# Kernel optimization log

Hardware: AMD Instinct MI355X
Metric: run time of the kernel (lower is better)

The kernel has to match this reference:

```python
import jax, jax.numpy as jnp
import numpy as np

NEG = -1e30  # safe -inf surrogate for log-space DP
BLANK = 0    # torch.nn.CTCLoss default blank index


def _ctc_loss_sum(lp, labels, in_lens, lab_lens):
    """CTC negative log-likelihood, summed over batch.
    lp: [T, B, V] log-probabilities; labels: [B, L] int; in_lens, lab_lens: [B] int.
    """
    T, B, V = lp.shape
    L = labels.shape[1]
    S = 2 * L + 1  # extended label length (blanks interleaved)
    s = jnp.arange(S)
    # extended label sequence z: blank at even positions, label at odd
    ext = jnp.where(s % 2 == 0, BLANK, labels[:, jnp.clip((s - 1) // 2, 0, L - 1)])  # [B,S]
    ext_m2 = jnp.concatenate([jnp.full((B, 2), BLANK, ext.dtype), ext[:, :-2]], axis=1)
    skip = (s >= 2) & (ext != BLANK) & (ext != ext_m2)  # [B,S] skip-transition allowed
    # emission log-probs gathered at extended labels: [T,B,S]
    emit = jnp.take_along_axis(lp, jnp.broadcast_to(ext[None], (T, B, S)), axis=2)
    alpha0 = jnp.full((B, S), NEG, lp.dtype)
    alpha0 = alpha0.at[:, 0].set(emit[0, :, 0]).at[:, 1].set(emit[0, :, 1])

    def step(alpha, inputs):
        emit_t, t = inputs
        a1 = jnp.concatenate([jnp.full((B, 1), NEG, alpha.dtype), alpha[:, :-1]], axis=1)
        a2 = jnp.concatenate([jnp.full((B, 2), NEG, alpha.dtype), alpha[:, :-2]], axis=1)
        comb = jnp.logaddexp(alpha, a1)
        comb = jnp.where(skip, jnp.logaddexp(comb, a2), comb)
        new = comb + emit_t
        # past each sequence's length, freeze alpha
        new = jnp.where(t < in_lens[:, None], new, alpha)
        return new, None

    alpha, _ = jax.lax.scan(step, alpha0, (emit[1:], jnp.arange(1, T)))
    s_last = 2 * lab_lens  # final blank position per sample
    bidx = jnp.arange(B)
    ll = jnp.logaddexp(alpha[bidx, s_last], alpha[bidx, s_last - 1])
    return jnp.sum(-ll)


def setup_inputs() -> dict:
    key = jax.random.key(0)
    k1, k2, k3, k4, k5, k6 = jax.random.split(key, 6)
    B, T, H, V, L = 16, 512, 512, 4096, 64
    hs_pad = jax.random.normal(k1, (B, T, H), dtype=jnp.float32)
    hs_lens = jax.random.randint(k2, (B,), T // 2, T + 1, dtype=jnp.int32)
    ys_pad = jax.random.randint(k3, (B, L), 1, V, dtype=jnp.int32)  # avoid blank=0
    ys_lens = jax.random.randint(k4, (B,), L // 2, L + 1, dtype=jnp.int32)
    W = jax.random.normal(k5, (H, V), dtype=jnp.float32) * (H ** -0.5)
    b = jax.random.normal(k6, (V,), dtype=jnp.float32) * 0.01
    return {"hs_pad": hs_pad, "hs_lens": hs_lens, "ys_pad": ys_pad,
            "ys_lens": ys_lens, "W": W, "b": b}


def reference(hs_pad, hs_lens, ys_pad, ys_lens, W, b):
    # projection (dropout_rate=0.0 -> identity) + log_softmax
    logits = jnp.einsum('bth,hv->btv', hs_pad, W) + b
    log_probs = jax.nn.log_softmax(logits, axis=-1)
    lp = jnp.transpose(log_probs, (1, 0, 2))  # [T,B,V]
    B = lp.shape[1]
    loss = _ctc_loss_sum(lp, ys_pad, hs_lens, ys_lens)
    return loss / B
```

## Files before the change

kernel.cpp:

```cpp
#include <hip/hip_runtime.h>
#include <hip/hip_bf16.h>
#include <math.h>

#define BB   16
#define TT   512
#define HH   512
#define VV   4096
#define LL   64
#define SS   129
#define JJ   65
#define MM   (BB*TT)

#define LOG2E 1.4426950408889634f
#define LN2   0.6931471805599453f

typedef __bf16 bf16;
typedef __attribute__((ext_vector_type(4))) __bf16 bf16x4;
typedef __attribute__((ext_vector_type(8))) __bf16 bf16x8;
typedef __attribute__((ext_vector_type(4))) float f32x4;

template<int CTRL>
__device__ __forceinline__ float dpp_mov(float x) {
    return __int_as_float(__builtin_amdgcn_update_dpp(
        __float_as_int(x), __float_as_int(x), CTRL, 0xF, 0xF, false));
}
__device__ __forceinline__ float row16_max(float x) {
    x = fmaxf(x, dpp_mov<0x128>(x));
    x = fmaxf(x, dpp_mov<0x124>(x));
    x = fmaxf(x, dpp_mov<0x122>(x));
    x = fmaxf(x, dpp_mov<0x121>(x));
    return x;
}
__device__ __forceinline__ float row16_sum(float x) {
    x += dpp_mov<0x128>(x);
    x += dpp_mov<0x124>(x);
    x += dpp_mov<0x122>(x);
    x += dpp_mov<0x121>(x);
    return x;
}
__device__ __forceinline__ float dpp_shr1_zero(float x) {
    int r = __builtin_amdgcn_update_dpp(0, __float_as_int(x),
                                        0x138 , 0xF, 0xF, false);
    return __int_as_float(r);
}
template<int CTRL>
__device__ __forceinline__ float dpp_max_t(float m) {
    int r = __builtin_amdgcn_update_dpp(0, __float_as_int(m), CTRL, 0xF, 0xF, false);
    return fmaxf(m, __int_as_float(r));
}

__global__ __launch_bounds__(256) void prep(const float* __restrict__ hs,
                                            const float* __restrict__ W,
                                            bf16* __restrict__ Abf,
                                            bf16* __restrict__ Wt)
{
    __shared__ float t[64][65];
    const int tid = threadIdx.x;
    int bx = blockIdx.x;
    if (bx < 4096) {
        int idx = bx * 256 + tid;
        float4 v = ((const float4*)hs)[idx];
        bf16x4 o = {(bf16)v.x, (bf16)v.y, (bf16)v.z, (bf16)v.w};
        *(bf16x4*)(Abf + (size_t)idx * 4) = o;
    } else {
        bx -= 4096;
        const int n0 = (bx & 63) * 64;
        const int k0 = (bx >> 6) * 64;
        #pragma unroll
        for (int i = 0; i < 16; ++i) {
            int idx = tid + i * 256;
            int kk = idx >> 6, nn = idx & 63;
            t[kk][nn] = W[(size_t)(k0 + kk) * VV + n0 + nn];
        }
        __syncthreads();
        #pragma unroll
        for (int i = 0; i < 16; ++i) {
            int idx = tid + i * 256;
            int nl = idx >> 6, kk = idx & 63;
            Wt[(size_t)(n0 + nl) * HH + k0 + kk] = (bf16)t[kk][nl];
        }
    }
}

#define TN 128
#define NT64 (VV / 64)

#define GLDS(src, dst) \
    __builtin_amdgcn_global_load_lds((const __attribute__((address_space(1))) void*)(src), \
                                     (__attribute__((address_space(3))) void*)(dst), 16, 0, 0)

__global__ __launch_bounds__(256) void gemm_lse_mfma(
    const bf16* __restrict__ A,
    const bf16* __restrict__ Bt,
    const float* __restrict__ bias,
    const int*  __restrict__ ys,
    float* __restrict__ part,
    float* __restrict__ glpT)
{
    __shared__ bf16 As[128 * 32];
    __shared__ bf16 Bs[128 * 32];
    const int tid = threadIdx.x;
    const int lane = tid & 63;
    const int wid = tid >> 6;
    const int wm = wid >> 1, wn = wid & 1;
    const int m0 = blockIdx.y * 128, n0 = blockIdx.x * 128;
    const int lq = lane & 15, kg = lane >> 4;

    f32x4 acc[4][4];
    const f32x4 z = {0.f, 0.f, 0.f, 0.f};
    #pragma unroll
    for (int i = 0; i < 4; ++i)
        #pragma unroll
        for (int j = 0; j < 4; ++j) acc[i][j] = z;

    const int c0 = tid;
    const int row0 = c0 >> 2, sl0 = (c0 & 3) ^ (row0 & 3);
    const int c1 = tid + 256;
    const int row1 = c1 >> 2, sl1 = (c1 & 3) ^ (row1 & 3);
    bf16* dstA0 = As + (size_t)(0 * 256 + (tid & 192)) * 8;
    bf16* dstA1 = As + (size_t)(1 * 256 + (tid & 192)) * 8;
    bf16* dstB0 = Bs + (size_t)(0 * 256 + (tid & 192)) * 8;
    bf16* dstB1 = Bs + (size_t)(1 * 256 + (tid & 192)) * 8;
    const bf16* srcA0 = A  + (size_t)(m0 + row0) * HH + sl0 * 8;
    const bf16* srcA1 = A  + (size_t)(m0 + row1) * HH + sl1 * 8;
    const bf16* srcB0 = Bt + (size_t)(n0 + row0) * HH + sl0 * 8;
    const bf16* srcB1 = Bt + (size_t)(n0 + row1) * HH + sl1 * 8;

    for (int k0 = 0; k0 < HH; k0 += 32) {
        GLDS(srcA0 + k0, dstA0);
        GLDS(srcA1 + k0, dstA1);
        GLDS(srcB0 + k0, dstB0);
        GLDS(srcB1 + k0, dstB1);
        __syncthreads();
        bf16x8 a[4], b[4];
        #pragma unroll
        for (int i = 0; i < 4; ++i) {
            int ar = wm * 64 + i * 16 + lq;
            a[i] = *(const bf16x8*)&As[ar * 32 + ((kg ^ (ar & 3)) * 8)];
        }
        #pragma unroll
        for (int j = 0; j < 4; ++j) {
            int br = wn * 64 + j * 16 + lq;
            b[j] = *(const bf16x8*)&Bs[br * 32 + ((kg ^ (br & 3)) * 8)];
        }
        #pragma unroll
        for (int i = 0; i < 4; ++i)
            #pragma unroll
            for (int j = 0; j < 4; ++j)
                acc[i][j] = __builtin_amdgcn_mfma_f32_16x16x32_bf16(a[i], b[j], acc[i][j], 0, 0, 0);
        __syncthreads();
    }

    const int ct = blockIdx.x * 2 + wn;
    float bj[4];
    #pragma unroll
    for (int j = 0; j < 4; ++j) bj[j] = bias[n0 + wn * 64 + j * 16 + lq];
    #pragma unroll
    for (int i = 0; i < 4; ++i) {
        #pragma unroll
        for (int r = 0; r < 4; ++r) {
            float v[4], mx = -3.4e38f;
            #pragma unroll
            for (int j = 0; j < 4; ++j) { v[j] = acc[i][j][r] + bj[j]; mx = fmaxf(mx, v[j]); }
            mx = row16_max(mx);
            float sm = 0.f;
            #pragma unroll
            for (int j = 0; j < 4; ++j) sm += __expf(v[j] - mx);
            sm = row16_sum(sm);
            if (lq == 0) {
                int rowg = m0 + wm * 64 + i * 16 + kg * 4 + r;
                size_t o = ((size_t)rowg * NT64 + ct) * 2;
                part[o] = mx; part[o + 1] = sm;
            }
        }
    }

    const int bidx = m0 >> 9;
    const int t0s  = (m0 & 511) + wm * 64;
    const int nbase = n0 + wn * 64;
    for (int j = 0; j < JJ; ++j) {
        int c = (j == 0) ? 0 : ys[bidx * LL + j - 1];
        int local = c - nbase;
        if (local >= 0 && local < 64) {
            int cl = local & 15;
            float bc = bias[c];
            #pragma unroll
            for (int jt = 0; jt < 4; ++jt) {
                if ((local >> 4) == jt && lq == cl) {
                    #pragma unroll
                    for (int i = 0; i < 4; ++i)
                        #pragma unroll
                        for (int r = 0; r < 4; ++r) {
                            int tt = t0s + i * 16 + kg * 4 + r;
                            glpT[(size_t)(bidx * JJ + j) * TT + tt] = acc[i][jt][r] + bc;
                        }
                }
            }
        }
    }
}

__global__ __launch_bounds__(256) void lse_merge(const float* __restrict__ part,
                                                 float* __restrict__ lse)
{
    const int lane = threadIdx.x & 63;
    const int r = blockIdx.x * 4 + (threadIdx.x >> 6);
    const float* p = part + (size_t)r * (NT64 * 2);
    float mx = p[2 * lane];
    float sm = p[2 * lane + 1];
    float wmax = mx;
    #pragma unroll
    for (int d = 1; d < 64; d <<= 1) wmax = fmaxf(wmax, __shfl_xor(wmax, d));
    float c = sm * __expf(mx - wmax);
    #pragma unroll
    for (int d = 1; d < 64; d <<= 1) c += __shfl_xor(c, d);
    if (lane == 0) lse[r] = wmax + logf(c);
}

#define F4AT(arr, u) ( ((u) & 3) == 0 ? arr[(u) >> 2].x \
                     : ((u) & 3) == 1 ? arr[(u) >> 2].y \
                     : ((u) & 3) == 2 ? arr[(u) >> 2].z : arr[(u) >> 2].w )

#define LOADI(p0v, pBv, blk) { \
    int bb_ = (blk); bb_ = bb_ < 32 ? bb_ : 31; \
    const float4* p0_ = (const float4*)(g0 + bb_ * 16); \
    const float4* pB_ = (const float4*)(gB + bb_ * 16); \
    p0v[0] = p0_[0]; p0v[1] = p0_[1]; p0v[2] = p0_[2]; p0v[3] = p0_[3]; \
    pBv[0] = pB_[0]; pBv[1] = pB_[1]; pBv[2] = pB_[2]; pBv[3] = pB_[3]; \
}

#define RVCOMP(rv, p0v, pBv, blk) { \
    const int tB_ = (blk) * 16; \
    _Pragma("unroll") \
    for (int u = 0; u < 16; ++u) { \
        rv[u] = __builtin_amdgcn_exp2f((F4AT(pBv, u) - F4AT(p0v, u)) * LOG2E); \
    } \
    if (tB_ > 0 && tB_ + 16 <= Tin) { \
        float s_ = 0.f; \
        _Pragma("unroll") \
        for (int u = 0; u < 16; ++u) s_ += F4AT(p0v, u); \
        corr += s_; \
    } else { \
        float s_ = 0.f; \
        _Pragma("unroll") \
        for (int u = 0; u < 16; ++u) { \
            int t_ = tB_ + u; \
            s_ += (t_ >= 1 && t_ < Tin) ? F4AT(p0v, u) : 0.f; \
        } \
        corr += s_; \
    } }

#define RESCALE() { \
        float m_ = fmaxf(fmaxf(vA ? A : 0.f, vB ? B : 0.f), vC ? C : 0.f); \
        m_ = dpp_max_t<0x111>(m_);  \
        m_ = dpp_max_t<0x112>(m_);  \
        m_ = dpp_max_t<0x114>(m_);  \
        m_ = dpp_max_t<0x118>(m_);  \
        m_ = dpp_max_t<0x142>(m_);  \
        m_ = dpp_max_t<0x143>(m_);  \
        int mb = __builtin_amdgcn_readlane(__float_as_int(m_), 63); \
        int k_ = ((mb >> 23) & 0xFF) - 127; \
        float sc = __int_as_float((127 - k_) << 23); \
        A *= sc; B *= sc; C *= sc; K += k_; \
    }

#define DO16N(rv, blk) { \
    const int tB_ = (blk) * 16; \
    if (tB_ > 0 && tB_ + 16 <= Tin) { \
        _Pragma("unroll") \
        for (int u = 0; u < 16; ++u) { \
            float prevB = dpp_shr1_zero(B); \
            float nA = A + prevB; \
            float t1 = A + B; \
            float t2 = skipB ? prevB : 0.f; \
            float nB = (t1 + t2) * rv[u]; \
            float nC = C + B; \
            A = nA; B = nB; C = nC; \
            if (u == 7 || u == 15) RESCALE(); \
        } \
    } else { \
        _Pragma("unroll") \
        for (int u = 0; u < 16; ++u) { \
            int t_ = tB_ + u; \
            bool upd = (t_ >= 1) && (t_ < Tin); \
            float prevB = dpp_shr1_zero(B); \
            float nA = A + prevB; \
            float t1 = A + B; \
            float t2 = skipB ? prevB : 0.f; \
            float nB = (t1 + t2) * rv[u]; \
            float nC = C + B; \
            A = upd ? nA : A; B = upd ? nB : B; C = upd ? nC : C; \
            if (u == 7 || u == 15) RESCALE(); \
        } \
    } }

__global__ __launch_bounds__(64) void ctc_dp(
    const float* __restrict__ glpT, const float* __restrict__ lse,
    const int* __restrict__ ys, const int* __restrict__ hs_lens,
    const int* __restrict__ ys_lens, float* __restrict__ nll)
{
    const int b = blockIdx.x;
    const int l = threadIdx.x;
    const float* g0 = glpT + (size_t)(b * JJ) * TT;
    const float* gB = glpT + (size_t)(b * JJ + l + 1) * TT;
    const float* ls = lse + (size_t)b * TT;
    const int Tin = hs_lens[b];
    const int Ll  = ys_lens[b];

    const bool vA = (l <= Ll);
    const bool vB = (l <  Ll);
    const bool vC = (l == 63) && (Ll == 64);

    int cc = ys[b * LL + l];
    bool skipB = false;
    if (l >= 1) { int cp = ys[b * LL + l - 1]; skipB = (cc != 0) && (cc != cp); }

    float raw0_0 = g0[0];
    float d0 = (gB[0] - raw0_0) * LOG2E;
    float A = (l == 0) ? 1.0f : 0.0f;
    float B = (l == 0) ? __builtin_amdgcn_exp2f(d0) : 0.0f;
    float C = 0.0f;
    float corr = raw0_0;
    int K = 0;

    float4 p0a[4], pBa[4], p0b[4], pBb[4];
    float rva[16], rvb[16];
    LOADI(p0a, pBa, 0);
    LOADI(p0b, pBb, 1);
    for (int blk = 0; blk < 32; blk += 2) {
        RVCOMP(rva, p0a, pBa, blk);
        LOADI(p0a, pBa, blk + 2);
        DO16N(rva, blk);
        RVCOMP(rvb, p0b, pBb, blk + 1);
        LOADI(p0b, pBb, blk + 3);
        DO16N(rvb, blk + 1);
        if (16 * (blk + 2) >= Tin) break;
    }

    float lsum = 0.f;
    for (int tt = l; tt < Tin; tt += 64) lsum += ls[tt];
    #pragma unroll
    for (int d = 1; d < 64; d <<= 1) lsum += __shfl_xor(lsum, d);

    float v1 = (Ll == 64) ? __shfl(C, 63, 64) : __shfl(A, Ll, 64);
    float v2 = __shfl(B, Ll - 1, 64);
    if (l == 0) {
        float ll2 = __builtin_amdgcn_logf(v1 + v2) + (float)K + (corr - lsum) * LOG2E;
        nll[b] = -ll2 * LN2;
    }
}

__global__ void finalize(const float* __restrict__ nll, float* __restrict__ out)
{
    float v = (threadIdx.x < BB) ? nll[threadIdx.x] : 0.f;
    #pragma unroll
    for (int d = 32; d >= 1; d >>= 1) v += __shfl_down(v, d);
    if (threadIdx.x == 0) out[0] = v / (float)BB;
}

extern "C" void kernel_launch(void* const* d_in, const int* in_sizes, int n_in,
                              void* d_out, int out_size, void* d_ws, size_t ws_size,
                              hipStream_t stream) {
    const float* hs      = (const float*)d_in[0];
    const int*   hs_lens = (const int*)  d_in[1];
    const int*   ys      = (const int*)  d_in[2];
    const int*   ys_lens = (const int*)  d_in[3];
    const float* W       = (const float*)d_in[4];
    const float* bias    = (const float*)d_in[5];
    float* out = (float*)d_out;

    float* ws   = (float*)d_ws;
    float* part = ws;
    float* lse  = part + (size_t)MM * NT64 * 2;
    float* glpT = lse  + MM;
    float* nll  = glpT + (size_t)BB * JJ * TT;
    bf16*  Abf  = (bf16*)(nll + 16);
    bf16*  Wt   = Abf + (size_t)MM * HH;

    prep<<<4608, 256, 0, stream>>>(hs, W, Abf, Wt);
    gemm_lse_mfma<<<dim3(VV / TN, MM / 128), 256, 0, stream>>>(Abf, Wt, bias, ys, part, glpT);
    lse_merge<<<MM / 4, 256, 0, stream>>>(part, lse);
    ctc_dp<<<BB, 64, 0, stream>>>(glpT, lse, ys, hs_lens, ys_lens, nll);
    finalize<<<1, 64, 0, stream>>>(nll, out);
}
```

Measured before the change: 187.3 us.

## Fuse LSE merge and finalize into CTC DP kernel with extra waves

Removes the separate lse_merge and finalize launches. The CTC DP now runs in wave 0 of a 256-thread block, while waves 1-3 merge the per-tile max/sum partials into log-sum-exp values and sum them over valid timesteps in parallel. The output is zeroed in prep, and each batch block adds its contribution with an atomicAdd, which removes the nll buffer and the extra kernel launches. In exchange, the LSE merge runs on only 16 blocks rather than 2048, so its reads from part may become the critical path if they take longer than the serial DP.

Result: faster. 183.2 us (-2.2%).

```diff
diff --git a/kernel.cpp b/kernel.cpp
--- a/kernel.cpp
+++ b/kernel.cpp
@@ -52,11 +52,13 @@
 __global__ __launch_bounds__(256) void prep(const float* __restrict__ hs,
                                             const float* __restrict__ W,
                                             bf16* __restrict__ Abf,
-                                            bf16* __restrict__ Wt)
+                                            bf16* __restrict__ Wt,
+                                            float* __restrict__ out)
 {
     __shared__ float t[64][65];
     const int tid = threadIdx.x;
     int bx = blockIdx.x;
+    if (bx == 0 && tid == 0) out[0] = 0.f;
     if (bx < 4096) {
         int idx = bx * 256 + tid;
         float4 v = ((const float4*)hs)[idx];
@@ -198,23 +200,6 @@
             }
         }
     }
-}
-
-__global__ __launch_bounds__(256) void lse_merge(const float* __restrict__ part,
-                                                 float* __restrict__ lse)
-{
-    const int lane = threadIdx.x & 63;
-    const int r = blockIdx.x * 4 + (threadIdx.x >> 6);
-    const float* p = part + (size_t)r * (NT64 * 2);
-    float mx = p[2 * lane];
-    float sm = p[2 * lane + 1];
-    float wmax = mx;
-    #pragma unroll
-    for (int d = 1; d < 64; d <<= 1) wmax = fmaxf(wmax, __shfl_xor(wmax, d));
-    float c = sm * __expf(mx - wmax);
-    #pragma unroll
-    for (int d = 1; d < 64; d <<= 1) c += __shfl_xor(c, d);
-    if (lane == 0) lse[r] = wmax + logf(c);
 }
 
 #define F4AT(arr, u) ( ((u) & 3) == 0 ? arr[(u) >> 2].x \
@@ -294,68 +279,84 @@
         } \
     } }
 
-__global__ __launch_bounds__(64) void ctc_dp(
-    const float* __restrict__ glpT, const float* __restrict__ lse,
+__global__ __launch_bounds__(256) void ctc_tail(
+    const float* __restrict__ glpT, const float* __restrict__ part,
     const int* __restrict__ ys, const int* __restrict__ hs_lens,
-    const int* __restrict__ ys_lens, float* __restrict__ nll)
+    const int* __restrict__ ys_lens, float* __restrict__ out)
 {
+    __shared__ float lsum_sh[4];
     const int b = blockIdx.x;
-    const int l = threadIdx.x;
-    const float* g0 = glpT + (size_t)(b * JJ) * TT;
-    const float* gB = glpT + (size_t)(b * JJ + l + 1) * TT;
-    const float* ls = lse + (size_t)b * TT;
+    const int tid = threadIdx.x;
+    const int wave = tid >> 6;
+    const int lane = tid & 63;
     const int Tin = hs_lens[b];
     const int Ll  = ys_lens[b];
 
-    const bool vA = (l <= Ll);
-    const bool vB = (l <  Ll);
-    const bool vC = (l == 63) && (Ll == 64);
-
-    int cc = ys[b * LL + l];
-    bool skipB = false;
-    if (l >= 1) { int cp = ys[b * LL + l - 1]; skipB = (cc != 0) && (cc != cp); }
-
-    float raw0_0 = g0[0];
-    float d0 = (gB[0] - raw0_0) * LOG2E;
-    float A = (l == 0) ? 1.0f : 0.0f;
-    float B = (l == 0) ? __builtin_amdgcn_exp2f(d0) : 0.0f;
-    float C = 0.0f;
-    float corr = raw0_0;
+    float v1 = 0.f, v2 = 0.f, corr = 0.f;
     int K = 0;
 
-    float4 p0a[4], pBa[4], p0b[4], pBb[4];
-    float rva[16], rvb[16];
-    LOADI(p0a, pBa, 0);
-    LOADI(p0b, pBb, 1);
-    for (int blk = 0; blk < 32; blk += 2) {
-        RVCOMP(rva, p0a, pBa, blk);
-        LOADI(p0a, pBa, blk + 2);
-        DO16N(rva, blk);
-        RVCOMP(rvb, p0b, pBb, blk + 1);
-        LOADI(p0b, pBb, blk + 3);
-        DO16N(rvb, blk + 1);
-        if (16 * (blk + 2) >= Tin) break;
-    }
-
-    float lsum = 0.f;
-    for (int tt = l; tt < Tin; tt += 64) lsum += ls[tt];
-    #pragma unroll
-    for (int d = 1; d < 64; d <<= 1) lsum += __shfl_xor(lsum, d);
-
-    float v1 = (Ll == 64) ? __shfl(C, 63, 64) : __shfl(A, Ll, 64);
-    float v2 = __shfl(B, Ll - 1, 64);
-    if (l == 0) {
-        float ll2 = __builtin_amdgcn_logf(v1 + v2) + (float)K + (corr - lsum) * LOG2E;
-        nll[b] = -ll2 * LN2;
-    }
-}
-
-__global__ void finalize(const float* __restrict__ nll, float* __restrict__ out)
-{
-    float v = (threadIdx.x < BB) ? nll[threadIdx.x] : 0.f;
-    #pragma unroll
-    for (int d = 32; d >= 1; d >>= 1) v += __shfl_down(v, d);
-    if (threadIdx.x == 0) out[0] = v / (float)BB;
+    if (wave == 0) {
+        const int l = lane;
+        const float* g0 = glpT + (size_t)(b * JJ) * TT;
+        const float* gB = glpT + (size_t)(b * JJ + l + 1) * TT;
+
+        const bool vA = (l <= Ll);
+        const bool vB = (l <  Ll);
+        const bool vC = (l == 63) && (Ll == 64);
+
+        int cc = ys[b * LL + l];
+        bool skipB = false;
+        if (l >= 1) { int cp = ys[b * LL + l - 1]; skipB = (cc != 0) && (cc != cp); }
+
+        float raw0_0 = g0[0];
+        float d0 = (gB[0] - raw0_0) * LOG2E;
+        float A = (l == 0) ? 1.0f : 0.0f;
+        float B = (l == 0) ? __builtin_amdgcn_exp2f(d0) : 0.0f;
+        float C = 0.0f;
+        corr = raw0_0;
+
+        float4 p0a[4], pBa[4], p0b[4], pBb[4];
+        float rva[16], rvb[16];
+        LOADI(p0a, pBa, 0);
+        LOADI(p0b, pBb, 1);
+        for (int blk = 0; blk < 32; blk += 2) {
+            RVCOMP(rva, p0a, pBa, blk);
+            LOADI(p0a, pBa, blk + 2);
+            DO16N(rva, blk);
+            RVCOMP(rvb, p0b, pBb, blk + 1);
+            LOADI(p0b, pBb, blk + 3);
+            DO16N(rvb, blk + 1);
+            if (16 * (blk + 2) >= Tin) break;
+        }
+
+        v1 = (Ll == 64) ? __shfl(C, 63, 64) : __shfl(A, Ll, 64);
+        v2 = __shfl(B, Ll - 1, 64);
+    } else {
+        const int t0 = (wave - 1) * 171;
+        const int t1 = (t0 + 171 < TT) ? (t0 + 171) : TT;
+        const int grp = lane >> 4, li = lane & 15;
+        float lsum = 0.f;
+        for (int t = t0 + grp; t < t1; t += 4) {
+            const float* p = part + ((size_t)(b * TT + t)) * (NT64 * 2) + li * 8;
+            float4 a  = ((const float4*)p)[0];
+            float4 c4 = ((const float4*)p)[1];
+            float ml = fmaxf(fmaxf(a.x, a.z), fmaxf(c4.x, c4.z));
+            float sl = a.y  * __expf(a.x  - ml) + a.w  * __expf(a.z  - ml)
+                     + c4.y * __expf(c4.x - ml) + c4.w * __expf(c4.z - ml);
+            float wm = row16_max(ml);
+            float ss = row16_sum(sl * __expf(ml - wm));
+            if (li == 0 && t < Tin) lsum += wm + logf(ss);
+        }
+        #pragma unroll
+        for (int d = 1; d < 64; d <<= 1) lsum += __shfl_xor(lsum, d);
+        if (lane == 0) lsum_sh[wave] = lsum;
+    }
+    __syncthreads();
+    if (tid == 0) {
+        float lsumT = lsum_sh[1] + lsum_sh[2] + lsum_sh[3];
+        float ll2 = __builtin_amdgcn_logf(v1 + v2) + (float)K + (corr - lsumT) * LOG2E;
+        atomicAdd(out, (-ll2 * LN2) * (1.0f / (float)BB));
+    }
 }
 
 extern "C" void kernel_launch(void* const* d_in, const int* in_sizes, int n_in,
@@ -371,15 +372,11 @@
 
     float* ws   = (float*)d_ws;
     float* part = ws;
-    float* lse  = part + (size_t)MM * NT64 * 2;
-    float* glpT = lse  + MM;
-    float* nll  = glpT + (size_t)BB * JJ * TT;
-    bf16*  Abf  = (bf16*)(nll + 16);
+    float* glpT = part + (size_t)MM * NT64 * 2;
+    bf16*  Abf  = (bf16*)(glpT + (size_t)BB * JJ * TT);
     bf16*  Wt   = Abf + (size_t)MM * HH;
 
-    prep<<<4608, 256, 0, stream>>>(hs, W, Abf, Wt);
+    prep<<<4608, 256, 0, stream>>>(hs, W, Abf, Wt, out);
     gemm_lse_mfma<<<dim3(VV / TN, MM / 128), 256, 0, stream>>>(Abf, Wt, bias, ys, part, glpT);
-    lse_merge<<<MM / 4, 256, 0, stream>>>(part, lse);
-    ctc_dp<<<BB, 64, 0, stream>>>(glpT, lse, ys, hs_lens, ys_lens, nll);
-    finalize<<<1, 64, 0, stream>>>(nll, out);
-}
+    ctc_tail<<<BB, 256, 0, stream>>>(glpT, part, ys, hs_lens, ys_lens, out);
+}
```
